# Kernel tuning notes

Hardware: AMD Instinct MI355X
Metric: run time of the kernel (lower is better)

Reference implementation:

```python
import jax, jax.numpy as jnp
from jax import lax
import numpy as np

B, T, NCLS, D = 64, 2048, 20, 2048
LCS_LEN, FSD_LEN = 64, 32
LAMB1, LAMB2, LAMB3 = 1.0, 5e-5, 8e-5
LAMB_LCS, LAMB_FSD = 0.01, 0.01
FEAT_MARGIN = 50.0
THRES = 0.5
GAMMA = 0.1


def cos_sim(a, b):
    a = a / jnp.linalg.norm(a, axis=1, keepdims=True)
    b = b / jnp.linalg.norm(b, axis=1, keepdims=True)
    return a @ b.T


def dp_fsd(c0, c1):
    # soft-LCS/DTW-style recurrence with maxGamma (soft max) over 3 neighbors
    h = c0.shape[-1] // 2
    m = cos_sim(c0[:, :h], c1[:, :h])  # [L, L]
    g = cos_sim(c0[:, h:], c1[:, h:])  # [L, L]
    L = m.shape[0]

    def row_step(prev_row, mg):
        m_row, g_row = mg
        diag = prev_row[:-1]  # C[i-1, j-1]
        up = prev_row[1:]     # C[i-1, j]

        def col_step(left, xs):  # left = C[i, j-1]
            d, u, mij, gij = xs
            neigh = jnp.stack([d, gij + u, gij + left])
            val = mij + GAMMA * jax.nn.logsumexp(neigh / GAMMA)
            return val, val

        _, row_vals = lax.scan(col_step, jnp.zeros((), m.dtype), (diag, up, m_row, g_row))
        new_row = jnp.concatenate([jnp.zeros((1,), m.dtype), row_vals])
        return new_row, None

    final_row, _ = lax.scan(row_step, jnp.zeros(L + 1, m.dtype), (m, g))
    return final_row[-1]


def dp_lcs(c0, c1):
    s = cos_sim(c0, c1)  # [L, L]
    L = s.shape[0]

    def row_step(prev_row, s_row):
        diag = prev_row[:-1]
        up = prev_row[1:]

        def col_step(left, xs):
            d, u, sij = xs
            val = jnp.where(sij > THRES, d + sij, jnp.maximum(u, left))
            return val, val

        _, row_vals = lax.scan(col_step, jnp.zeros((), s.dtype), (diag, up, s_row))
        return jnp.concatenate([jnp.zeros((1,), s.dtype), row_vals]), None

    final_row, _ = lax.scan(row_step, jnp.zeros(L + 1, s.dtype), s)
    return final_row[-1]


def cls_criterion(p, lab):
    return -jnp.mean(jnp.sum(jnp.log(p + 1e-10) * lab, axis=1))


def forward_once(ai_cls, ac_cls, ab_cls, vlab, att, ai_feat, ac_feat, ab_feat, ai_cas):
    bs = ai_cls.shape[0]
    ones = jnp.ones((bs, 1), ai_cls.dtype)
    zeros = jnp.zeros((bs, 1), ai_cls.dtype)
    inst_lab = jnp.concatenate([vlab, zeros], axis=1)
    cont_lab = jnp.concatenate([vlab, ones], axis=1)
    back_lab = jnp.concatenate([jnp.zeros_like(vlab), ones], axis=1)
    inst_lab = inst_lab / jnp.sum(inst_lab, axis=1, keepdims=True)
    cont_lab = cont_lab / jnp.sum(cont_lab, axis=1, keepdims=True)
    back_lab = back_lab / jnp.sum(back_lab, axis=1, keepdims=True)

    inst_loss = cls_criterion(ai_cls, inst_lab)
    cont_loss = cls_criterion(ac_cls, cont_lab)
    back_loss = cls_criterion(ab_cls, back_lab)

    guide_loss = jnp.mean(jnp.sum(jnp.abs(1.0 - ai_cas[:, :, -1] - lax.stop_gradient(att[:, :, 0])), axis=1))

    n_inst = jnp.linalg.norm(ai_feat, axis=1)
    n_cont = jnp.linalg.norm(ac_feat, axis=1)
    n_back = jnp.linalg.norm(ab_feat, axis=1)
    f1 = jnp.maximum(FEAT_MARGIN - n_inst + n_cont, 0.0)
    f2 = jnp.maximum(FEAT_MARGIN - n_cont + n_back, 0.0)
    f3 = n_back
    feat_loss = jnp.mean((f1 + f2 + f3) ** 2)

    sparse_loss = jnp.mean(jnp.sum(att[:, :, :2], axis=1))

    cls_loss = inst_loss + cont_loss + back_loss  # THUMOS14 weights 1/1/1
    return cls_loss + LAMB1 * guide_loss + LAMB2 * feat_loss + LAMB3 * sparse_loss


def _pair_loss(vals, pair_label):
    bs = vals.shape[0]
    pos = jnp.sum(vals * pair_label)
    neg = jnp.sum(vals * (1.0 - pair_label))
    pos_num = jnp.sum(pair_label)
    neg_num = bs - pos_num
    return neg / (neg_num + 1e-10) - pos / (pos_num + 1e-10)


def ftcl_forward(act_inst_cls_0, act_cont_cls_0, act_back_cls_0, vid_label_0, temp_att_0,
                 act_inst_feat_0, act_cont_feat_0, act_back_feat_0, act_inst_cas_0,
                 lcs_candi_0, fsd_act_candi_0, fsd_bak_candi_0,
                 act_inst_cls_1, act_cont_cls_1, act_back_cls_1, vid_label_1, temp_att_1,
                 act_inst_feat_1, act_cont_feat_1, act_back_feat_1, act_inst_cas_1,
                 lcs_candi_1, fsd_act_candi_1, fsd_bak_candi_1):
    loss_0 = forward_once(act_inst_cls_0, act_cont_cls_0, act_back_cls_0, vid_label_0, temp_att_0,
                          act_inst_feat_0, act_cont_feat_0, act_back_feat_0, act_inst_cas_0)
    loss_1 = forward_once(act_inst_cls_1, act_cont_cls_1, act_back_cls_1, vid_label_1, temp_att_1,
                          act_inst_feat_1, act_cont_feat_1, act_back_feat_1, act_inst_cas_1)
    acm_loss = (loss_0 + loss_1) / 2.0

    pair_label = (jnp.sum(vid_label_0 * vid_label_1, axis=1) > 0).astype(jnp.float32)  # [B]

    lcs = jax.vmap(dp_lcs)(lcs_candi_0, lcs_candi_1)  # [B]
    lcs_loss = _pair_loss(lcs, pair_label)

    # pair==1 -> act_1, pair==0 -> bak_1 (matches the per-sample branch in torch)
    fsd_c1 = jnp.where(pair_label[:, None, None] > 0, fsd_act_candi_1, fsd_bak_candi_1)
    fsd = jax.vmap(dp_fsd)(fsd_act_candi_0, fsd_c1)  # [B]
    fsd_loss = _pair_loss(fsd, pair_label)

    return acm_loss + LAMB_LCS * lcs_loss + LAMB_FSD * fsd_loss


def setup_inputs() -> dict:
    key = jax.random.key(0)
    ks = iter(jax.random.split(key, 32))
    rand = lambda s: jax.random.uniform(next(ks), s, jnp.float32)
    randn = lambda s: jax.random.normal(next(ks), s, jnp.float32)
    inp = {}
    for sfx in ('0', '1'):
        inp[f'act_inst_cls_{sfx}'] = rand((B, NCLS + 1))
        inp[f'act_cont_cls_{sfx}'] = rand((B, NCLS + 1))
        inp[f'act_back_cls_{sfx}'] = rand((B, NCLS + 1))
        inp[f'vid_label_{sfx}'] = jnp.ones((B, NCLS), jnp.float32)
        inp[f'temp_att_{sfx}'] = rand((B, T, 3))
        inp[f'act_inst_feat_{sfx}'] = randn((B, D))
        inp[f'act_cont_feat_{sfx}'] = randn((B, D))
        inp[f'act_back_feat_{sfx}'] = randn((B, D))
        inp[f'act_inst_cas_{sfx}'] = rand((B, T, NCLS + 1))
        inp[f'lcs_candi_{sfx}'] = randn((B, LCS_LEN, D))
        inp[f'fsd_act_candi_{sfx}'] = randn((B, FSD_LEN, D))
        inp[f'fsd_bak_candi_{sfx}'] = randn((B, FSD_LEN, D))
    return inp


def reference(act_inst_cls_0, act_cont_cls_0, act_back_cls_0, vid_label_0, temp_att_0,
              act_inst_feat_0, act_cont_feat_0, act_back_feat_0, act_inst_cas_0,
              lcs_candi_0, fsd_act_candi_0, fsd_bak_candi_0,
              act_inst_cls_1, act_cont_cls_1, act_back_cls_1, vid_label_1, temp_att_1,
              act_inst_feat_1, act_cont_feat_1, act_back_feat_1, act_inst_cas_1,
              lcs_candi_1, fsd_act_candi_1, fsd_bak_candi_1):
    return ftcl_forward(act_inst_cls_0, act_cont_cls_0, act_back_cls_0, vid_label_0, temp_att_0,
                        act_inst_feat_0, act_cont_feat_0, act_back_feat_0, act_inst_cas_0,
                        lcs_candi_0, fsd_act_candi_0, fsd_bak_candi_0,
                        act_inst_cls_1, act_cont_cls_1, act_back_cls_1, vid_label_1, temp_att_1,
                        act_inst_feat_1, act_cont_feat_1, act_back_feat_1, act_inst_cas_1,
                        lcs_candi_1, fsd_act_candi_1, fsd_bak_candi_1)
```

## Files before the change

kernel.cpp:

```cpp
#include <hip/hip_runtime.h>
#include <math.h>

#define Bn 64
#define Tn 2048
#define NCLS 20
#define Dn 2048
#define LCSL 64
#define FSDL 32

typedef __bf16 bf16x4 __attribute__((ext_vector_type(4)));
typedef __bf16 bf16x8 __attribute__((ext_vector_type(8)));
typedef float f32x4 __attribute__((ext_vector_type(4)));

#define WS_LCS 0
#define WS_FSD 64
#define WS_NORM 128
#define WS_GS 512
#define WS_LSQ 1024
#define WS_FSQ 66560
#define WS_SPART 99328
#define WS_MG 2196480

__global__ __launch_bounds__(256) void mega_kernel(
    const float* __restrict__ lcs0, const float* __restrict__ lcs1,
    const float* __restrict__ fA0, const float* __restrict__ fA1,
    const float* __restrict__ fB1,
    const float* __restrict__ vid0, const float* __restrict__ vid1,
    const float* __restrict__ cas0, const float* __restrict__ att0,
    const float* __restrict__ cas1, const float* __restrict__ att1,
    const float* __restrict__ f0, const float* __restrict__ f1,
    const float* __restrict__ f2, const float* __restrict__ f3,
    const float* __restrict__ f4, const float* __restrict__ f5,
    float* __restrict__ ws) {
    __shared__ __align__(16) __bf16 tA[64 * 256];
    __shared__ __align__(16) __bf16 tB[64 * 256];
    const int t = threadIdx.x;
    const int bid = blockIdx.x;
    const int w = t >> 6, lane = t & 63;
    const int quad = lane >> 4, l16 = lane & 15;

    if (bid < 512) {
        const int b = bid >> 3, ks = bid & 7;
        const float* c0 = lcs0 + (size_t)b * LCSL * Dn + ks * 256;
        const float* c1 = lcs1 + (size_t)b * LCSL * Dn + ks * 256;

        float4 pA[16], pB[16];
        #pragma unroll
        for (int r = 0; r < 16; ++r)
            pA[r] = *(const float4*)(c0 + (size_t)(w * 16 + r) * Dn + lane * 4);
        #pragma unroll
        for (int r = 0; r < 16; ++r)
            pB[r] = *(const float4*)(c1 + (size_t)(w * 16 + r) * Dn + lane * 4);

        float* qsq = ws + WS_LSQ + (size_t)(b * 8 + ks) * 128;
        #pragma unroll
        for (int r = 0; r < 16; ++r) {
            int rr = w * 16 + r;
            float4 av = pA[r];
            bf16x4 a4 = {(__bf16)av.x, (__bf16)av.y, (__bf16)av.z, (__bf16)av.w};
            int c = (lane >> 1) ^ (rr & 7);
            *(bf16x4*)&tA[rr * 256 + (c << 3) + ((lane & 1) << 2)] = a4;
            float sa = av.x * av.x + av.y * av.y + av.z * av.z + av.w * av.w;
            #pragma unroll
            for (int m = 1; m < 64; m <<= 1) sa += __shfl_xor(sa, m);
            if (lane == 0) qsq[rr] = sa;
        }
        #pragma unroll
        for (int r = 0; r < 16; ++r) {
            int rr = w * 16 + r;
            float4 bv = pB[r];
            bf16x4 b4 = {(__bf16)bv.x, (__bf16)bv.y, (__bf16)bv.z, (__bf16)bv.w};
            int c = (lane >> 1) ^ (rr & 7);
            *(bf16x4*)&tB[rr * 256 + (c << 3) + ((lane & 1) << 2)] = b4;
            float sb = bv.x * bv.x + bv.y * bv.y + bv.z * bv.z + bv.w * bv.w;
            #pragma unroll
            for (int m = 1; m < 64; m <<= 1) sb += __shfl_xor(sb, m);
            if (lane == 0) qsq[64 + rr] = sb;
        }
        __syncthreads();

        f32x4 acc[4] = {};
        const int ar = w * 16 + l16;
        #pragma unroll
        for (int s = 0; s < 8; ++s) {
            bf16x8 af = *(const bf16x8*)&tA[ar * 256 + ((((s * 4 + quad) ^ (ar & 7))) << 3)];
            #pragma unroll
            for (int tj = 0; tj < 4; ++tj) {
                int br = tj * 16 + l16;
                bf16x8 bf = *(const bf16x8*)&tB[br * 256 + ((((s * 4 + quad) ^ (br & 7))) << 3)];
                acc[tj] = __builtin_amdgcn_mfma_f32_16x16x32_bf16(af, bf, acc[tj], 0, 0, 0);
            }
        }
        float* dst = ws + WS_SPART + (size_t)(b * 8 + ks) * 4096;
        #pragma unroll
        for (int tj = 0; tj < 4; ++tj)
            #pragma unroll
            for (int rg = 0; rg < 4; ++rg)
                dst[(w * 16 + quad * 4 + rg) * 64 + tj * 16 + l16] = acc[tj][rg];
    } else if (bid < 1024) {
        const int qb = bid - 512;
        const int b = qb >> 3, half = (qb >> 2) & 1, ks = qb & 3;
        float ps = 0.f;
        for (int c = 0; c < NCLS; ++c) ps += vid0[b * NCLS + c] * vid1[b * NCLS + c];
        const float* base1 = (ps > 0.f) ? fA1 : fB1;
        const float* c0 = fA0 + (size_t)b * FSDL * Dn + half * 1024 + ks * 256;
        const float* c1 = base1 + (size_t)b * FSDL * Dn + half * 1024 + ks * 256;

        float4 pA[8], pB[8];
        #pragma unroll
        for (int r = 0; r < 8; ++r)
            pA[r] = *(const float4*)(c0 + (size_t)(w * 8 + r) * Dn + lane * 4);
        #pragma unroll
        for (int r = 0; r < 8; ++r)
            pB[r] = *(const float4*)(c1 + (size_t)(w * 8 + r) * Dn + lane * 4);

        float* qsq = ws + WS_FSQ + (size_t)((b * 2 + half) * 4 + ks) * 64;
        #pragma unroll
        for (int r = 0; r < 8; ++r) {
            int rr = w * 8 + r;
            float4 av = pA[r];
            bf16x4 a4 = {(__bf16)av.x, (__bf16)av.y, (__bf16)av.z, (__bf16)av.w};
            int c = (lane >> 1) ^ (rr & 7);
            *(bf16x4*)&tA[rr * 256 + (c << 3) + ((lane & 1) << 2)] = a4;
            float sa = av.x * av.x + av.y * av.y + av.z * av.z + av.w * av.w;
            #pragma unroll
            for (int m = 1; m < 64; m <<= 1) sa += __shfl_xor(sa, m);
            if (lane == 0) qsq[rr] = sa;
        }
        #pragma unroll
        for (int r = 0; r < 8; ++r) {
            int rr = w * 8 + r;
            float4 bv = pB[r];
            bf16x4 b4 = {(__bf16)bv.x, (__bf16)bv.y, (__bf16)bv.z, (__bf16)bv.w};
            int c = (lane >> 1) ^ (rr & 7);
            *(bf16x4*)&tB[rr * 256 + (c << 3) + ((lane & 1) << 2)] = b4;
            float sb = bv.x * bv.x + bv.y * bv.y + bv.z * bv.z + bv.w * bv.w;
            #pragma unroll
            for (int m = 1; m < 64; m <<= 1) sb += __shfl_xor(sb, m);
            if (lane == 0) qsq[32 + rr] = sb;
        }
        __syncthreads();

        const int wi = w >> 1, wj = w & 1;
        const int ar = wi * 16 + l16, br = wj * 16 + l16;
        f32x4 acc = {};
        #pragma unroll
        for (int s = 0; s < 8; ++s) {
            bf16x8 af = *(const bf16x8*)&tA[ar * 256 + ((((s * 4 + quad) ^ (ar & 7))) << 3)];
            bf16x8 bf = *(const bf16x8*)&tB[br * 256 + ((((s * 4 + quad) ^ (br & 7))) << 3)];
            acc = __builtin_amdgcn_mfma_f32_16x16x32_bf16(af, bf, acc, 0, 0, 0);
        }
        float* dst = ws + WS_MG + (size_t)((b * 2 + half) * 4 + ks) * 1024;
        #pragma unroll
        for (int rg = 0; rg < 4; ++rg)
            dst[(wi * 16 + quad * 4 + rg) * 32 + wj * 16 + l16] = acc[rg];
    } else if (bid < 1152) {
        const int gb = bid - 1024;
        const int N = Bn * Tn;
        float g0 = 0.f, s0 = 0.f, g1 = 0.f, s1 = 0.f;
        for (int n = gb * 256 + t; n < 2 * N; n += 128 * 256) {
            int sfx = (n >= N);
            int m = sfx ? (n - N) : n;
            const float* cas = sfx ? cas1 : cas0;
            const float* att = sfx ? att1 : att0;
            float a0 = att[m * 3 + 0];
            float a1 = att[m * 3 + 1];
            float g = fabsf(1.0f - cas[m * (NCLS + 1) + NCLS] - a0);
            float s = a0 + a1;
            if (sfx) { g1 += g; s1 += s; } else { g0 += g; s0 += s; }
        }
        float* red = (float*)tA;
        float vals[4] = {g0, s0, g1, s1};
        #pragma unroll
        for (int v = 0; v < 4; ++v) red[v * 256 + t] = vals[v];
        __syncthreads();
        for (int o = 128; o; o >>= 1) {
            if (t < o) {
                #pragma unroll
                for (int v = 0; v < 4; ++v) red[v * 256 + t] += red[v * 256 + t + o];
            }
            __syncthreads();
        }
        if (t < 4) ws[WS_GS + gb * 4 + t] = red[t * 256];
    } else {
        int R = (bid - 1152) * 4 + w;
        const float* arr[6] = {f0, f1, f2, f3, f4, f5};
        const float* p = arr[R >> 6] + (size_t)(R & 63) * Dn;
        float s = 0.f;
        #pragma unroll
        for (int qd = 0; qd < 8; ++qd) {
            float4 v = *(const float4*)(p + qd * 256 + lane * 4);
            s += v.x * v.x + v.y * v.y + v.z * v.z + v.w * v.w;
        }
        for (int off = 32; off; off >>= 1) s += __shfl_down(s, off);
        if (lane == 0) ws[WS_NORM + R] = sqrtf(s);
    }
}

__global__ __launch_bounds__(256) void dp_kernel(float* __restrict__ ws) {
    const int t = threadIdx.x;
    if (blockIdx.x < 64) {
        const int b = blockIdx.x;
        __shared__ float S[64 * 68];
        __shared__ float inv[128];
        if (t < 128) {
            float s = 0.f;
            #pragma unroll
            for (int ks = 0; ks < 8; ++ks)
                s += ws[WS_LSQ + (size_t)(b * 8 + ks) * 128 + t];
            inv[t] = 1.0f / sqrtf(s);
        }
        __syncthreads();
        const float* sp = ws + WS_SPART + (size_t)b * 32768;
        #pragma unroll
        for (int qd = 0; qd < 4; ++qd) {
            int idx4 = qd * 256 + t;
            int i = idx4 >> 4, j = (idx4 & 15) * 4;
            float4 v = {0.f, 0.f, 0.f, 0.f};
            #pragma unroll
            for (int ks = 0; ks < 8; ++ks) {
                float4 p = *(const float4*)(sp + (size_t)ks * 4096 + idx4 * 4);
                v.x += p.x; v.y += p.y; v.z += p.z; v.w += p.w;
            }
            float ri = inv[i];
            S[i * 68 + j + 0] = v.x * ri * inv[64 + j + 0];
            S[i * 68 + j + 1] = v.y * ri * inv[64 + j + 1];
            S[i * 68 + j + 2] = v.z * ri * inv[64 + j + 2];
            S[i * 68 + j + 3] = v.w * ri * inv[64 + j + 3];
        }
        __syncthreads();
        if (t < 64) {
            float prev = 0.f, prevprev = 0.f;
            float sval_next = S[t * 68 + 0];
            for (int d = 2; d <= 128; ++d) {
                float s = sval_next;
                int jn = d - t - 1;
                if (jn >= 0 && jn < 64) sval_next = S[t * 68 + jn];
                float up = __shfl_up(prev, 1);
                float dg = __shfl_up(prevprev, 1);
                if (t == 0) { up = 0.f; dg = 0.f; }
                int j = d - t - 1;
                float left = prev;
                float val = (s > 0.5f) ? (dg + s) : fmaxf(up, left);
                float cur = (j >= 1 && j <= 64) ? val : 0.f;
                prevprev = prev;
                prev = cur;
            }
            if (t == 63) ws[WS_LCS + b] = prev;
        }
    } else {
        const int b = blockIdx.x - 64;
        __shared__ float M[32 * 36], G[32 * 36];
        __shared__ float inv[128];
        if (t < 128) {
            int half = t >> 6, sub = t & 63;
            float s = 0.f;
            #pragma unroll
            for (int ks = 0; ks < 4; ++ks)
                s += ws[WS_FSQ + (size_t)((b * 2 + half) * 4 + ks) * 64 + sub];
            inv[t] = 1.0f / sqrtf(s);
        }
        __syncthreads();
        {
            int idx4 = t;
            int i = idx4 >> 3, j = (idx4 & 7) * 4;
            float4 vM = {0.f, 0.f, 0.f, 0.f}, vG = {0.f, 0.f, 0.f, 0.f};
            #pragma unroll
            for (int ks = 0; ks < 4; ++ks) {
                float4 pM = *(const float4*)(ws + WS_MG + (size_t)((b * 2 + 0) * 4 + ks) * 1024 + idx4 * 4);
                float4 pG = *(const float4*)(ws + WS_MG + (size_t)((b * 2 + 1) * 4 + ks) * 1024 + idx4 * 4);
                vM.x += pM.x; vM.y += pM.y; vM.z += pM.z; vM.w += pM.w;
                vG.x += pG.x; vG.y += pG.y; vG.z += pG.z; vG.w += pG.w;
            }
            float riM = inv[i], riG = inv[64 + i];
            M[i * 36 + j + 0] = vM.x * riM * inv[32 + j + 0];
            M[i * 36 + j + 1] = vM.y * riM * inv[32 + j + 1];
            M[i * 36 + j + 2] = vM.z * riM * inv[32 + j + 2];
            M[i * 36 + j + 3] = vM.w * riM * inv[32 + j + 3];
            G[i * 36 + j + 0] = vG.x * riG * inv[96 + j + 0];
            G[i * 36 + j + 1] = vG.y * riG * inv[96 + j + 1];
            G[i * 36 + j + 2] = vG.z * riG * inv[96 + j + 2];
            G[i * 36 + j + 3] = vG.w * riG * inv[96 + j + 3];
        }
        __syncthreads();
        if (t < 32) {
            float prev = 0.f, prevprev = 0.f;
            float m_next = M[t * 36 + 0], g_next = G[t * 36 + 0];
            for (int d = 2; d <= 64; ++d) {
                float m = m_next, g = g_next;
                int jn = d - t - 1;
                if (jn >= 0 && jn < 32) { m_next = M[t * 36 + jn]; g_next = G[t * 36 + jn]; }
                float up = __shfl_up(prev, 1);
                float dg = __shfl_up(prevprev, 1);
                if (t == 0) { up = 0.f; dg = 0.f; }
                int j = d - t - 1;
                float left = prev;
                float x0 = dg * 10.0f;
                float x1 = (g + up) * 10.0f;
                float x2 = (g + left) * 10.0f;
                float mx = fmaxf(x0, fmaxf(x1, x2));
                float lse = mx + __logf(__expf(x0 - mx) + __expf(x1 - mx) + __expf(x2 - mx));
                float val = m + 0.1f * lse;
                float cur = (j >= 1 && j <= 32) ? val : 0.f;
                prevprev = prev;
                prev = cur;
            }
            if (t == 31) ws[WS_FSD + b] = prev;
        }
    }
}

__device__ float block_reduce(float v, float* red, int t) {
    red[t] = v;
    __syncthreads();
    for (int o = 128; o; o >>= 1) {
        if (t < o) red[t] += red[t + o];
        __syncthreads();
    }
    float r = red[0];
    __syncthreads();
    return r;
}

__global__ __launch_bounds__(256) void final_kernel(
    const float* __restrict__ ai0, const float* __restrict__ ac0,
    const float* __restrict__ ab0, const float* __restrict__ vid0,
    const float* __restrict__ ai1, const float* __restrict__ ac1,
    const float* __restrict__ ab1, const float* __restrict__ vid1,
    const float* __restrict__ ws, float* __restrict__ out) {
    __shared__ float rs0[Bn], rs1[Bn], plsh[Bn];
    __shared__ float red[256];
    int t = threadIdx.x;
    if (t < Bn) {
        float s0 = 0.f, s1 = 0.f, pp = 0.f;
        for (int c = 0; c < NCLS; ++c) {
            float a = vid0[t * NCLS + c], bl = vid1[t * NCLS + c];
            s0 += a; s1 += bl; pp += a * bl;
        }
        rs0[t] = s0;
        rs1[t] = s1;
        plsh[t] = (pp > 0.f) ? 1.f : 0.f;
    }
    __syncthreads();

    float inst0 = 0.f, cont0 = 0.f, back0 = 0.f;
    float inst1 = 0.f, cont1 = 0.f, back1 = 0.f;
    for (int idx = t; idx < Bn * (NCLS + 1); idx += 256) {
        int b = idx / (NCLS + 1), c = idx % (NCLS + 1);
        float v0 = (c < NCLS) ? vid0[b * NCLS + c] : 0.f;
        float v1 = (c < NCLS) ? vid1[b * NCLS + c] : 0.f;
        float wI0 = (c < NCLS) ? (v0 / rs0[b]) : 0.f;
        float wC0 = ((c < NCLS) ? v0 : 1.f) / (rs0[b] + 1.f);
        float wI1 = (c < NCLS) ? (v1 / rs1[b]) : 0.f;
        float wC1 = ((c < NCLS) ? v1 : 1.f) / (rs1[b] + 1.f);
        inst0 += logf(ai0[idx] + 1e-10f) * wI0;
        cont0 += logf(ac0[idx] + 1e-10f) * wC0;
        inst1 += logf(ai1[idx] + 1e-10f) * wI1;
        cont1 += logf(ac1[idx] + 1e-10f) * wC1;
        if (c == NCLS) {
            back0 += logf(ab0[idx] + 1e-10f);
            back1 += logf(ab1[idx] + 1e-10f);
        }
    }
    float sInst0 = block_reduce(inst0, red, t);
    float sCont0 = block_reduce(cont0, red, t);
    float sBack0 = block_reduce(back0, red, t);
    float sInst1 = block_reduce(inst1, red, t);
    float sCont1 = block_reduce(cont1, red, t);
    float sBack1 = block_reduce(back1, red, t);

    float g0 = 0.f, s0v = 0.f, g1 = 0.f, s1v = 0.f;
    for (int i = t; i < 128; i += 256) {
        g0  += ws[WS_GS + i * 4 + 0];
        s0v += ws[WS_GS + i * 4 + 1];
        g1  += ws[WS_GS + i * 4 + 2];
        s1v += ws[WS_GS + i * 4 + 3];
    }
    float sG0 = block_reduce(g0, red, t);
    float sS0 = block_reduce(s0v, red, t);
    float sG1 = block_reduce(g1, red, t);
    float sS1 = block_reduce(s1v, red, t);

    float fv0 = 0.f, fv1 = 0.f;
    if (t < Bn) {
        const float* nm = ws + WS_NORM;
        {
            float ni = nm[0 * Bn + t], nc = nm[1 * Bn + t], nb = nm[2 * Bn + t];
            float f1 = fmaxf(50.0f - ni + nc, 0.f);
            float f2 = fmaxf(50.0f - nc + nb, 0.f);
            float f = f1 + f2 + nb;
            fv0 = f * f;
        }
        {
            float ni = nm[3 * Bn + t], nc = nm[4 * Bn + t], nb = nm[5 * Bn + t];
            float f1 = fmaxf(50.0f - ni + nc, 0.f);
            float f2 = fmaxf(50.0f - nc + nb, 0.f);
            float f = f1 + f2 + nb;
            fv1 = f * f;
        }
    }
    float sFeat0 = block_reduce(fv0, red, t) / (float)Bn;
    float sFeat1 = block_reduce(fv1, red, t) / (float)Bn;

    float posL = 0.f, negL = 0.f, posF = 0.f, negF = 0.f, pln = 0.f;
    if (t < Bn) {
        float pl = plsh[t];
        float lv = ws[WS_LCS + t];
        float fv = ws[WS_FSD + t];
        posL = lv * pl; negL = lv * (1.f - pl);
        posF = fv * pl; negF = fv * (1.f - pl);
        pln = pl;
    }
    float sPosL = block_reduce(posL, red, t);
    float sNegL = block_reduce(negL, red, t);
    float sPosF = block_reduce(posF, red, t);
    float sNegF = block_reduce(negF, red, t);
    float sPln = block_reduce(pln, red, t);

    if (t == 0) {
        float cls0 = -(sInst0 + sCont0 + sBack0) / (float)Bn;
        float cls1 = -(sInst1 + sCont1 + sBack1) / (float)Bn;
        float guide0 = sG0 / (float)Bn;
        float sparse0 = sS0 / (float)(Bn * 2);
        float guide1 = sG1 / (float)Bn;
        float sparse1 = sS1 / (float)(Bn * 2);
        float loss0 = cls0 + 1.0f * guide0 + 5e-05f * sFeat0 + 8e-05f * sparse0;
        float loss1 = cls1 + 1.0f * guide1 + 5e-05f * sFeat1 + 8e-05f * sparse1;
        float acm = 0.5f * (loss0 + loss1);
        float posn = sPln;
        float negn = (float)Bn - posn;
        float lcs_loss = sNegL / (negn + 1e-10f) - sPosL / (posn + 1e-10f);
        float fsd_loss = sNegF / (negn + 1e-10f) - sPosF / (posn + 1e-10f);
        out[0] = acm + 0.01f * lcs_loss + 0.01f * fsd_loss;
    }
}

extern "C" void kernel_launch(void* const* d_in, const int* in_sizes, int n_in,
                              void* d_out, int out_size, void* d_ws, size_t ws_size,
                              hipStream_t stream) {
    (void)in_sizes; (void)n_in; (void)out_size; (void)ws_size;
    const float* ai0  = (const float*)d_in[0];
    const float* ac0  = (const float*)d_in[1];
    const float* ab0  = (const float*)d_in[2];
    const float* vid0 = (const float*)d_in[3];
    const float* att0 = (const float*)d_in[4];
    const float* fi0  = (const float*)d_in[5];
    const float* fc0  = (const float*)d_in[6];
    const float* fb0  = (const float*)d_in[7];
    const float* cas0 = (const float*)d_in[8];
    const float* lcs0 = (const float*)d_in[9];
    const float* fsdA0 = (const float*)d_in[10];
    const float* ai1  = (const float*)d_in[12];
    const float* ac1  = (const float*)d_in[13];
    const float* ab1  = (const float*)d_in[14];
    const float* vid1 = (const float*)d_in[15];
    const float* att1 = (const float*)d_in[16];
    const float* fi1  = (const float*)d_in[17];
    const float* fc1  = (const float*)d_in[18];
    const float* fb1  = (const float*)d_in[19];
    const float* cas1 = (const float*)d_in[20];
    const float* lcs1 = (const float*)d_in[21];
    const float* fsdA1 = (const float*)d_in[22];
    const float* fsdB1 = (const float*)d_in[23];

    float* ws = (float*)d_ws;

    mega_kernel<<<1248, 256, 0, stream>>>(lcs0, lcs1, fsdA0, fsdA1, fsdB1,
                                          vid0, vid1, cas0, att0, cas1, att1,
                                          fi0, fc0, fb0, fi1, fc1, fb1, ws);
    dp_kernel<<<128, 256, 0, stream>>>(ws);
    final_kernel<<<1, 256, 0, stream>>>(ai0, ac0, ab0, vid0, ai1, ac1, ab1, vid1, ws,
                                        (float*)d_out);
}
```

Baseline: 241.7 us.

## Load MFMA operands directly from global memory, dropping LDS staging tiles

The LCS and FSD cosine-similarity GEMM blocks now read their fp32 operands straight from global memory in the MFMA fragment layout and convert them to bf16 in registers. This removes the two 32KB shared tiles, the swizzled LDS writes and the block barrier. Squared norms are accumulated alongside with fewer shuffles. Shared memory shrinks to a 4KB reduction buffer and launch bounds request 4 blocks per CU to raise occupancy. The cost is that B rows are reloaded by all four waves in the LCS path, and the global accesses become strided 32-byte row reads that coalesce less well than the old full-row loads.

```diff
diff --git a/kernel.cpp b/kernel.cpp
--- a/kernel.cpp
+++ b/kernel.cpp
@@ -8,7 +8,6 @@
 #define LCSL 64
 #define FSDL 32
 
-typedef __bf16 bf16x4 __attribute__((ext_vector_type(4)));
 typedef __bf16 bf16x8 __attribute__((ext_vector_type(8)));
 typedef float f32x4 __attribute__((ext_vector_type(4)));
 
@@ -21,7 +20,16 @@
 #define WS_SPART 99328
 #define WS_MG 2196480
 
-__global__ __launch_bounds__(256) void mega_kernel(
+__device__ __forceinline__ bf16x8 cvt8(float4 a, float4 b) {
+    bf16x8 r = {(__bf16)a.x, (__bf16)a.y, (__bf16)a.z, (__bf16)a.w,
+                (__bf16)b.x, (__bf16)b.y, (__bf16)b.z, (__bf16)b.w};
+    return r;
+}
+__device__ __forceinline__ float dot4(float4 a) {
+    return a.x * a.x + a.y * a.y + a.z * a.z + a.w * a.w;
+}
+
+__global__ __launch_bounds__(256, 4) void mega_kernel(
     const float* __restrict__ lcs0, const float* __restrict__ lcs1,
     const float* __restrict__ fA0, const float* __restrict__ fA1,
     const float* __restrict__ fB1,
@@ -32,8 +40,7 @@
     const float* __restrict__ f2, const float* __restrict__ f3,
     const float* __restrict__ f4, const float* __restrict__ f5,
     float* __restrict__ ws) {
-    __shared__ __align__(16) __bf16 tA[64 * 256];
-    __shared__ __align__(16) __bf16 tB[64 * 256];
+    __shared__ float red[1024];
     const int t = threadIdx.x;
     const int bid = blockIdx.x;
     const int w = t >> 6, lane = t & 63;
@@ -43,52 +50,40 @@
         const int b = bid >> 3, ks = bid & 7;
         const float* c0 = lcs0 + (size_t)b * LCSL * Dn + ks * 256;
         const float* c1 = lcs1 + (size_t)b * LCSL * Dn + ks * 256;
-
-        float4 pA[16], pB[16];
-        #pragma unroll
-        for (int r = 0; r < 16; ++r)
-            pA[r] = *(const float4*)(c0 + (size_t)(w * 16 + r) * Dn + lane * 4);
-        #pragma unroll
-        for (int r = 0; r < 16; ++r)
-            pB[r] = *(const float4*)(c1 + (size_t)(w * 16 + r) * Dn + lane * 4);
-
+        const int ar = w * 16 + l16;
+        const float* arow = c0 + (size_t)ar * Dn;
+
+        f32x4 acc[4] = {};
+        float sqa = 0.f;
+        float sqb[4] = {0.f, 0.f, 0.f, 0.f};
+        #pragma unroll
+        for (int s = 0; s < 8; ++s) {
+            const int ko = s * 32 + quad * 8;
+            float4 a0 = *(const float4*)(arow + ko);
+            float4 a1 = *(const float4*)(arow + ko + 4);
+            sqa += dot4(a0) + dot4(a1);
+            bf16x8 af = cvt8(a0, a1);
+            #pragma unroll
+            for (int tj = 0; tj < 4; ++tj) {
+                const float* brow = c1 + (size_t)(tj * 16 + l16) * Dn;
+                float4 b0 = *(const float4*)(brow + ko);
+                float4 b1 = *(const float4*)(brow + ko + 4);
+                if (w == 0) sqb[tj] += dot4(b0) + dot4(b1);
+                bf16x8 bfr = cvt8(b0, b1);
+                acc[tj] = __builtin_amdgcn_mfma_f32_16x16x32_bf16(af, bfr, acc[tj], 0, 0, 0);
+            }
+        }
         float* qsq = ws + WS_LSQ + (size_t)(b * 8 + ks) * 128;
-        #pragma unroll
-        for (int r = 0; r < 16; ++r) {
-            int rr = w * 16 + r;
-            float4 av = pA[r];
-            bf16x4 a4 = {(__bf16)av.x, (__bf16)av.y, (__bf16)av.z, (__bf16)av.w};
-            int c = (lane >> 1) ^ (rr & 7);
-            *(bf16x4*)&tA[rr * 256 + (c << 3) + ((lane & 1) << 2)] = a4;
-            float sa = av.x * av.x + av.y * av.y + av.z * av.z + av.w * av.w;
-            #pragma unroll
-            for (int m = 1; m < 64; m <<= 1) sa += __shfl_xor(sa, m);
-            if (lane == 0) qsq[rr] = sa;
-        }
-        #pragma unroll
-        for (int r = 0; r < 16; ++r) {
-            int rr = w * 16 + r;
-            float4 bv = pB[r];
-            bf16x4 b4 = {(__bf16)bv.x, (__bf16)bv.y, (__bf16)bv.z, (__bf16)bv.w};
-            int c = (lane >> 1) ^ (rr & 7);
-            *(bf16x4*)&tB[rr * 256 + (c << 3) + ((lane & 1) << 2)] = b4;
-            float sb = bv.x * bv.x + bv.y * bv.y + bv.z * bv.z + bv.w * bv.w;
-            #pragma unroll
-            for (int m = 1; m < 64; m <<= 1) sb += __shfl_xor(sb, m);
-            if (lane == 0) qsq[64 + rr] = sb;
-        }
-        __syncthreads();
-
-        f32x4 acc[4] = {};
-        const int ar = w * 16 + l16;
-        #pragma unroll
-        for (int s = 0; s < 8; ++s) {
-            bf16x8 af = *(const bf16x8*)&tA[ar * 256 + ((((s * 4 + quad) ^ (ar & 7))) << 3)];
+        sqa += __shfl_xor(sqa, 16);
+        sqa += __shfl_xor(sqa, 32);
+        if (lane < 16) qsq[ar] = sqa;
+        if (w == 0) {
             #pragma unroll
             for (int tj = 0; tj < 4; ++tj) {
-                int br = tj * 16 + l16;
-                bf16x8 bf = *(const bf16x8*)&tB[br * 256 + ((((s * 4 + quad) ^ (br & 7))) << 3)];
-                acc[tj] = __builtin_amdgcn_mfma_f32_16x16x32_bf16(af, bf, acc[tj], 0, 0, 0);
+                float sb = sqb[tj];
+                sb += __shfl_xor(sb, 16);
+                sb += __shfl_xor(sb, 32);
+                if (lane < 16) qsq[64 + tj * 16 + l16] = sb;
             }
         }
         float* dst = ws + WS_SPART + (size_t)(b * 8 + ks) * 4096;
@@ -105,51 +100,31 @@
         const float* base1 = (ps > 0.f) ? fA1 : fB1;
         const float* c0 = fA0 + (size_t)b * FSDL * Dn + half * 1024 + ks * 256;
         const float* c1 = base1 + (size_t)b * FSDL * Dn + half * 1024 + ks * 256;
-
-        float4 pA[8], pB[8];
-        #pragma unroll
-        for (int r = 0; r < 8; ++r)
-            pA[r] = *(const float4*)(c0 + (size_t)(w * 8 + r) * Dn + lane * 4);
-        #pragma unroll
-        for (int r = 0; r < 8; ++r)
-            pB[r] = *(const float4*)(c1 + (size_t)(w * 8 + r) * Dn + lane * 4);
-
-        float* qsq = ws + WS_FSQ + (size_t)((b * 2 + half) * 4 + ks) * 64;
-        #pragma unroll
-        for (int r = 0; r < 8; ++r) {
-            int rr = w * 8 + r;
-            float4 av = pA[r];
-            bf16x4 a4 = {(__bf16)av.x, (__bf16)av.y, (__bf16)av.z, (__bf16)av.w};
-            int c = (lane >> 1) ^ (rr & 7);
-            *(bf16x4*)&tA[rr * 256 + (c << 3) + ((lane & 1) << 2)] = a4;
-            float sa = av.x * av.x + av.y * av.y + av.z * av.z + av.w * av.w;
-            #pragma unroll
-            for (int m = 1; m < 64; m <<= 1) sa += __shfl_xor(sa, m);
-            if (lane == 0) qsq[rr] = sa;
-        }
-        #pragma unroll
-        for (int r = 0; r < 8; ++r) {
-            int rr = w * 8 + r;
-            float4 bv = pB[r];
-            bf16x4 b4 = {(__bf16)bv.x, (__bf16)bv.y, (__bf16)bv.z, (__bf16)bv.w};
-            int c = (lane >> 1) ^ (rr & 7);
-            *(bf16x4*)&tB[rr * 256 + (c << 3) + ((lane & 1) << 2)] = b4;
-            float sb = bv.x * bv.x + bv.y * bv.y + bv.z * bv.z + bv.w * bv.w;
-            #pragma unroll
-            for (int m = 1; m < 64; m <<= 1) sb += __shfl_xor(sb, m);
-            if (lane == 0) qsq[32 + rr] = sb;
-        }
-        __syncthreads();
-
         const int wi = w >> 1, wj = w & 1;
         const int ar = wi * 16 + l16, br = wj * 16 + l16;
+        const float* arow = c0 + (size_t)ar * Dn;
+        const float* brow = c1 + (size_t)br * Dn;
+
         f32x4 acc = {};
+        float sqa = 0.f, sqbv = 0.f;
         #pragma unroll
         for (int s = 0; s < 8; ++s) {
-            bf16x8 af = *(const bf16x8*)&tA[ar * 256 + ((((s * 4 + quad) ^ (ar & 7))) << 3)];
-            bf16x8 bf = *(const bf16x8*)&tB[br * 256 + ((((s * 4 + quad) ^ (br & 7))) << 3)];
-            acc = __builtin_amdgcn_mfma_f32_16x16x32_bf16(af, bf, acc, 0, 0, 0);
-        }
+            const int ko = s * 32 + quad * 8;
+            float4 a0 = *(const float4*)(arow + ko);
+            float4 a1 = *(const float4*)(arow + ko + 4);
+            float4 b0 = *(const float4*)(brow + ko);
+            float4 b1 = *(const float4*)(brow + ko + 4);
+            sqa += dot4(a0) + dot4(a1);
+            sqbv += dot4(b0) + dot4(b1);
+            acc = __builtin_amdgcn_mfma_f32_16x16x32_bf16(cvt8(a0, a1), cvt8(b0, b1), acc, 0, 0, 0);
+        }
+        float* qsq = ws + WS_FSQ + (size_t)((b * 2 + half) * 4 + ks) * 64;
+        sqa += __shfl_xor(sqa, 16);
+        sqa += __shfl_xor(sqa, 32);
+        if (wj == 0 && lane < 16) qsq[ar] = sqa;
+        sqbv += __shfl_xor(sqbv, 16);
+        sqbv += __shfl_xor(sqbv, 32);
+        if (wi == 0 && lane < 16) qsq[32 + br] = sqbv;
         float* dst = ws + WS_MG + (size_t)((b * 2 + half) * 4 + ks) * 1024;
         #pragma unroll
         for (int rg = 0; rg < 4; ++rg)
@@ -169,7 +144,6 @@
             float s = a0 + a1;
             if (sfx) { g1 += g; s1 += s; } else { g0 += g; s0 += s; }
         }
-        float* red = (float*)tA;
         float vals[4] = {g0, s0, g1, s1};
         #pragma unroll
         for (int v = 0; v < 4; ++v) red[v * 256 + t] = vals[v];
@@ -190,7 +164,7 @@
         #pragma unroll
         for (int qd = 0; qd < 8; ++qd) {
             float4 v = *(const float4*)(p + qd * 256 + lane * 4);
-            s += v.x * v.x + v.y * v.y + v.z * v.z + v.w * v.w;
+            s += dot4(v);
         }
         for (int off = 32; off; off >>= 1) s += __shfl_down(s, off);
         if (lane == 0) ws[WS_NORM + R] = sqrtf(s);
```

After: 250.5 us. +3.6%, slower.
